# Optimization experiments

Hardware: AMD Instinct MI355X
Metric: run time of the kernel (lower is better)

## Reference

```python
import jax, jax.numpy as jnp
import numpy as np

# Multi-level grid resolutions (module constants from init_kwargs)
RESO_3D = [16, 32, 64]
RESO_2D = [64, 128, 256]
EPS = 1e-9


def _corners(D):
    # binary corner offsets, shape (2**D, D)
    c = np.stack(np.meshgrid(*([np.arange(2)] * D), indexing='ij'), axis=-1).reshape(-1, D)
    return jnp.asarray(c, dtype=jnp.int32)


def _coords_weights(xyz, reso):
    # xyz in [0,1), shape (N, D). Returns flat voxel idx (N, 2**D) and trilinear weights (N, 2**D).
    D = xyz.shape[1]
    corners = _corners(D)                                   # (C, D)
    x = xyz * (reso - 1)
    x0 = jnp.floor(x)
    frac = x - x0                                           # (N, D)
    x0 = x0.astype(jnp.int32)
    cc = jnp.clip(x0[:, None, :] + corners[None], 0, reso - 1)   # (N, C, D)
    w = jnp.prod(jnp.where(corners[None] == 1, frac[:, None, :], 1.0 - frac[:, None, :]), axis=-1)  # (N, C)
    strides = (reso ** jnp.arange(D - 1, -1, -1)).astype(jnp.int32)  # row-major
    idx = jnp.sum(cc * strides, axis=-1)                    # (N, C)
    return idx, w


def _grid_create(xyz, feat, reso):
    # Scatter-splat: weighted-average point features into a dense level grid (reso**D, F).
    N, D = xyz.shape
    F = feat.shape[1]
    idx, w = _coords_weights(xyz, reso)                     # (N, C)
    flat_idx = idx.reshape(-1)
    wf = jnp.zeros((reso ** D, F), dtype=feat.dtype).at[flat_idx].add(
        (w[..., None] * feat[:, None, :]).reshape(-1, F))
    ws = jnp.zeros((reso ** D,), dtype=feat.dtype).at[flat_idx].add(w.reshape(-1))
    return wf / jnp.maximum(ws, EPS)[:, None]


def _grid_encode(xyz, grid, reso):
    # Gather + trilinear interpolation from a dense level grid. Returns (M, F).
    idx, w = _coords_weights(xyz, reso)                     # (M, C)
    vals = grid[idx]                                        # (M, C, F)
    return jnp.sum(w[..., None] * vals, axis=1)


def _spatial_ctx(xyz_c, xyz_i, feat):
    outs = []
    # 3D multi-level grid
    for R in RESO_3D:
        g = _grid_create(xyz_c, feat, R)
        outs.append(_grid_encode(xyz_i, g, R))
    # triplane 2D grids: xy, xz, yz
    for dims in ((0, 1), (0, 2), (1, 2)):
        xc = xyz_c[:, list(dims)]
        xi = xyz_i[:, list(dims)]
        for R in RESO_2D:
            g = _grid_create(xc, feat, R)
            outs.append(_grid_encode(xi, g, R))
    return jnp.concatenate(outs, axis=-1)  # (M, (L3 + 3*L2) * F)


def setup_inputs() -> dict:
    key = jax.random.key(0)
    k1, k2, k3 = jax.random.split(key, 3)
    N, M, F = 200000, 100000, 32
    xyz_for_creater = jax.random.uniform(k1, (N, 3), dtype=jnp.float32)
    xyz_for_interp = jax.random.uniform(k2, (M, 3), dtype=jnp.float32)
    feature = jax.random.normal(k3, (N, F), dtype=jnp.float32)
    return {"xyz_for_creater": xyz_for_creater,
            "xyz_for_interp": xyz_for_interp,
            "feature": feature}


def reference(xyz_for_creater, xyz_for_interp, feature):
    return _spatial_ctx(xyz_for_creater, xyz_for_interp, feature)
```

## Files before the change

kernel.cpp:

```cpp
#include <hip/hip_runtime.h>

#define NF 32
#define EPSF 1e-9f

#define KSORT 458752
#define VO16 0
#define VO32 4096
#define VO64Q 36864
#define VO128Q 49152
#define KVIS2 98304
#define KO16 0
#define KO32 4096
#define KO64 36864
#define KO64Q 299008
#define KO128Q 311296
#define KO256Q 360448
#define KVIS 557056

__device__ __forceinline__ int cell_coord(float xv, int R, float& fr) {
  float x = xv * (float)(R - 1);
  int i0 = (int)floorf(x);
  i0 = min(max(i0, 0), R - 2);
  fr = x - (float)i0;
  return i0;
}
__device__ __forceinline__ float bf2f(unsigned short u) {
  return __uint_as_float((unsigned)u << 16);
}
__device__ __forceinline__ unsigned short f2bf(float x) {
  unsigned b = __float_as_uint(x);
  return (unsigned short)((b + 0x7FFF + ((b >> 16) & 1)) >> 16);
}
__device__ __forceinline__ unsigned p1b2(unsigned x) {
  x &= 0x3FF;
  x = (x | (x << 16)) & 0x030000FF;
  x = (x | (x << 8)) & 0x0300F00F;
  x = (x | (x << 4)) & 0x030C30C3;
  x = (x | (x << 2)) & 0x09249249;
  return x;
}
__device__ __forceinline__ unsigned p1b1(unsigned x) {
  x &= 0xFFFF;
  x = (x | (x << 8)) & 0x00FF00FF;
  x = (x | (x << 4)) & 0x0F0F0F0F;
  x = (x | (x << 2)) & 0x33333333;
  x = (x | (x << 1)) & 0x55555555;
  return x;
}
__device__ __forceinline__ unsigned c1b2(unsigned x) {
  x &= 0x09249249u;
  x = (x | (x >> 2)) & 0x030C30C3u;
  x = (x | (x >> 4)) & 0x0300F00Fu;
  x = (x | (x >> 8)) & 0x030000FFu;
  x = (x | (x >> 16)) & 0x3FFu;
  return x;
}
__device__ __forceinline__ unsigned c1b1(unsigned x) {
  x &= 0x55555555u;
  x = (x | (x >> 1)) & 0x33333333u;
  x = (x | (x >> 2)) & 0x0F0F0F0Fu;
  x = (x | (x >> 4)) & 0x00FF00FFu;
  x = (x | (x >> 8)) & 0xFFFFu;
  return x;
}

__device__ __forceinline__ int xcd_swz(int bid, int n) {
  return (bid & 7) * (n >> 3) + (bid >> 3);
}

__device__ __forceinline__ void agg_hist(int key, int* cnt) {
  int lane = threadIdx.x & 63;
  unsigned long long amask = __ballot(1);
  int nact = __popcll(amask);
  int prev = __shfl_up(key, 1);
  bool leader = (lane == 0) || (prev != key);
  unsigned long long lmask = __ballot(leader);
  if (leader) {
    unsigned long long above = (lane < 63) ? (lmask >> (lane + 1)) : 0ULL;
    int next = above ? (lane + 1 + (__ffsll((unsigned long long)above) - 1)) : nact;
    atomicAdd(&cnt[key], next - lane);
  }
}
template <int NC>
__device__ __forceinline__ void agg_place_batch(const int (&key)[NC], int* cur,
                                                int (&pos)[NC]) {
  int lane = threadIdx.x & 63;
  unsigned long long amask = __ballot(1);
  int nact = __popcll(amask);
  int ret[NC];
  int lp[NC];
#pragma unroll
  for (int c = 0; c < NC; ++c) {
    int prev = __shfl_up(key[c], 1);
    bool leader = (lane == 0) || (prev != key[c]);
    unsigned long long lmask = __ballot(leader);
    unsigned long long below = lmask & ((2ULL << lane) - 1ULL);
    lp[c] = 63 - __clzll((long long)below);
    ret[c] = 0;
    if (leader) {
      unsigned long long above = (lane < 63) ? (lmask >> (lane + 1)) : 0ULL;
      int next = above ? (lane + 1 + (__ffsll((unsigned long long)above) - 1)) : nact;
      ret[c] = atomicAdd(&cur[key[c]], next - lane);
    }
  }
#pragma unroll
  for (int c = 0; c < NC; ++c) pos[c] = __shfl(ret[c], lp[c]) + (lane - lp[c]);
}

__global__ __launch_bounds__(256) void sort_hist_all(
    const float* __restrict__ xyz, int* __restrict__ cnt, int N) {
  int p = blockIdx.x * blockDim.x + threadIdx.x;
  if (p >= N) return;
  float fr;
  int c64[3], c256[3];
#pragma unroll
  for (int d = 0; d < 3; ++d) {
    c64[d] = cell_coord(xyz[p * 3 + d], 64, fr);
    c256[d] = cell_coord(xyz[p * 3 + d], 256, fr);
  }
  int k3 = (int)((p1b2((unsigned)c64[0]) << 2) | (p1b2((unsigned)c64[1]) << 1) |
                 p1b2((unsigned)c64[2]));
  atomicAdd(&cnt[k3], 1);
#pragma unroll
  for (int g = 0; g < 3; ++g) {
    int a = (g < 2) ? 0 : 1, b = (g == 0) ? 1 : 2;
    int key = 262144 + g * 65536 +
              (int)((p1b1((unsigned)c256[a]) << 1) | p1b1((unsigned)c256[b]));
    atomicAdd(&cnt[key], 1);
  }
}
__global__ __launch_bounds__(256) void sort_place_all(
    const float* __restrict__ xyz, int* __restrict__ cur, int* __restrict__ perm, int N) {
  int p = blockIdx.x * blockDim.x + threadIdx.x;
  if (p >= N) return;
  float fr;
  int c64[3], c256[3];
#pragma unroll
  for (int d = 0; d < 3; ++d) {
    c64[d] = cell_coord(xyz[p * 3 + d], 64, fr);
    c256[d] = cell_coord(xyz[p * 3 + d], 256, fr);
  }
  int k3 = (int)((p1b2((unsigned)c64[0]) << 2) | (p1b2((unsigned)c64[1]) << 1) |
                 p1b2((unsigned)c64[2]));
  perm[atomicAdd(&cur[k3], 1)] = p;
#pragma unroll
  for (int g = 0; g < 3; ++g) {
    int a = (g < 2) ? 0 : 1, b = (g == 0) ? 1 : 2;
    int key = 262144 + g * 65536 +
              (int)((p1b1((unsigned)c256[a]) << 1) | p1b1((unsigned)c256[b]));
    perm[atomicAdd(&cur[key], 1)] = p;
  }
}
__global__ __launch_bounds__(256) void permute_all(
    const float* __restrict__ xyz, const float* __restrict__ feat,
    const int* __restrict__ perm, float* __restrict__ xyz_s,
    unsigned short* __restrict__ feat_s, float* __restrict__ xy_g,
    unsigned short* __restrict__ feat_g, int N) {
  int t = blockIdx.x * blockDim.x + threadIdx.x;
  int s = t >> 5, f = t & 31;
  if (s >= 4 * N) return;
  int q = perm[s];
  float v = feat[(size_t)q * NF + f];
  if (s < N) {
    feat_s[(size_t)s * NF + f] = f2bf(v);
    if (f < 3) xyz_s[s * 3 + f] = xyz[q * 3 + f];
  } else {
    int sl = s - N;
    int g = sl / N;
    feat_g[(size_t)sl * NF + f] = f2bf(v);
    if (f < 2) {
      int a = (g < 2) ? 0 : 1, b = (g == 0) ? 1 : 2;
      xy_g[(size_t)sl * 2 + f] = xyz[q * 3 + (f == 0 ? a : b)];
    }
  }
}

__global__ __launch_bounds__(256) void scan_blocksum(
    const int* __restrict__ cnt, int* __restrict__ bsum, int K) {
  __shared__ int red[256];
  int base = blockIdx.x * 2048 + threadIdx.x * 8;
  int s = 0;
#pragma unroll
  for (int j = 0; j < 8; ++j) {
    int k = base + j;
    if (k < K) s += cnt[k];
  }
  red[threadIdx.x] = s;
  __syncthreads();
  for (int off = 128; off > 0; off >>= 1) {
    if (threadIdx.x < off) red[threadIdx.x] += red[threadIdx.x + off];
    __syncthreads();
  }
  if (threadIdx.x == 0) bsum[blockIdx.x] = red[0];
}
__global__ __launch_bounds__(256) void scan_write(
    const int* __restrict__ cnt, const int* __restrict__ bsum,
    int* __restrict__ cur, int K) {
  __shared__ int lds[256];
  __shared__ int boff;
  int b = blockIdx.x, t = threadIdx.x;
  if (t == 0) {
    int s = 0;
    for (int j = 0; j < b; ++j) s += bsum[j];
    boff = s;
  }
  int base = b * 2048 + t * 8;
  int v[8];
  int s = 0;
#pragma unroll
  for (int j = 0; j < 8; ++j) {
    int k = base + j;
    v[j] = (k < K) ? cnt[k] : 0;
    s += v[j];
  }
  lds[t] = s;
  __syncthreads();
  for (int off = 1; off < 256; off <<= 1) {
    int add = (t >= off) ? lds[t - off] : 0;
    __syncthreads();
    lds[t] += add;
    __syncthreads();
  }
  int run = boff + lds[t] - s;
#pragma unroll
  for (int j = 0; j < 8; ++j) {
    int k = base + j;
    if (k < K) {
      cur[k] = run;
      run += v[j];
    }
  }
}

__global__ __launch_bounds__(256) void hist_fused(
    const float* __restrict__ xyz_s, const float* __restrict__ xy_g,
    int* __restrict__ cnt, int N) {
  int y = blockIdx.y;
  int p = blockIdx.x * blockDim.x + threadIdx.x;
  if (p >= N) return;
  if (y < 2) {
    int R = 16 << y;
    int ko = (y == 0) ? VO16 : VO32;
    unsigned a0[3], a1[3];
    float fr[3];
#pragma unroll
    for (int d = 0; d < 3; ++d) {
      int i0 = cell_coord(xyz_s[p * 3 + d], R, fr[d]);
      a0[d] = p1b2((unsigned)i0);
      a1[d] = p1b2((unsigned)(i0 + 1));
    }
#pragma unroll
    for (int cb = 0; cb < 8; ++cb) {
      unsigned key = 0;
#pragma unroll
      for (int d = 0; d < 3; ++d) {
        int o = (cb >> d) & 1;
        key |= (o ? a1[d] : a0[d]) << (2 - d);
      }
      agg_hist(ko + (int)key, cnt);
    }
  } else {
    int idx = y - 2;
    int g = idx >> 1, r = idx & 1;
    int sl = g * N + p;
    int R = 64 << r;
    int kb = (r == 0) ? VO64Q : VO128Q;
    int base = kb + g * R * R;
    float frx, fry;
    int ix = cell_coord(xy_g[(size_t)sl * 2 + 0], R, frx);
    int iy = cell_coord(xy_g[(size_t)sl * 2 + 1], R, fry);
    unsigned ax0 = p1b1((unsigned)ix), ax1 = p1b1((unsigned)(ix + 1));
    unsigned ay0 = p1b1((unsigned)iy), ay1 = p1b1((unsigned)(iy + 1));
#pragma unroll
    for (int cb = 0; cb < 4; ++cb) {
      int o0 = (cb >> 1) & 1, o1 = cb & 1;
      agg_hist(base + (int)(((o0 ? ax1 : ax0) << 1) | (o1 ? ay1 : ay0)), cnt);
    }
  }
}

__global__ __launch_bounds__(256) void place_fused(
    const float* __restrict__ xyz_s, const float* __restrict__ xy_g,
    int* __restrict__ cur_v, int2* __restrict__ visits, int N) {
  int y = blockIdx.y;
  int p = blockIdx.x * blockDim.x + threadIdx.x;
  if (p >= N) return;
  if (y < 2) {
    int R = 16 << y;
    int ko = (y == 0) ? VO16 : VO32;
    unsigned a0[3], a1[3];
    float fr[3];
#pragma unroll
    for (int d = 0; d < 3; ++d) {
      int i0 = cell_coord(xyz_s[p * 3 + d], R, fr[d]);
      a0[d] = p1b2((unsigned)i0);
      a1[d] = p1b2((unsigned)(i0 + 1));
    }
    int keys[8];
    float ws[8];
#pragma unroll
    for (int cb = 0; cb < 8; ++cb) {
      float w = 1.f;
      unsigned key = 0;
#pragma unroll
      for (int d = 0; d < 3; ++d) {
        int o = (cb >> d) & 1;
        w *= o ? fr[d] : (1.f - fr[d]);
        key |= (o ? a1[d] : a0[d]) << (2 - d);
      }
      keys[cb] = ko + (int)key;
      ws[cb] = w;
    }
    int pos[8];
    agg_place_batch<8>(keys, cur_v, pos);
#pragma unroll
    for (int cb = 0; cb < 8; ++cb)
      visits[pos[cb]] = make_int2(p, __float_as_int(ws[cb]));
  } else {
    int idx = y - 2;
    int g = idx >> 1, r = idx & 1;
    int sl = g * N + p;
    int R = 64 << r;
    int kb = (r == 0) ? VO64Q : VO128Q;
    int base = kb + g * R * R;
    float frx, fry;
    int ix = cell_coord(xy_g[(size_t)sl * 2 + 0], R, frx);
    int iy = cell_coord(xy_g[(size_t)sl * 2 + 1], R, fry);
    unsigned ax0 = p1b1((unsigned)ix), ax1 = p1b1((unsigned)(ix + 1));
    unsigned ay0 = p1b1((unsigned)iy), ay1 = p1b1((unsigned)(iy + 1));
    int keys[4];
    float ws[4];
#pragma unroll
    for (int cb = 0; cb < 4; ++cb) {
      int o0 = (cb >> 1) & 1, o1 = cb & 1;
      ws[cb] = (o0 ? frx : 1.f - frx) * (o1 ? fry : 1.f - fry);
      keys[cb] = base + (int)(((o0 ? ax1 : ax0) << 1) | (o1 ? ay1 : ay0));
    }
    int pos[4];
    agg_place_batch<4>(keys, cur_v, pos);
#pragma unroll
    for (int cb = 0; cb < 4; ++cb)
      visits[pos[cb]] = make_int2(sl, __float_as_int(ws[cb]));
  }
}

__global__ __launch_bounds__(256) void create_block_fused(
    const unsigned short* __restrict__ feat_s, const unsigned short* __restrict__ feat_g,
    const int* __restrict__ cnt, const int* __restrict__ cur_end,
    const int2* __restrict__ visits, unsigned short* __restrict__ grid) {
  __shared__ int2 vlds[1024];
  __shared__ float2 lacc[256];
  __shared__ float lw[16];
  int bid = blockIdx.x;
  int vo, go, base, nseg;
  const unsigned short* feat;
  if (bid < 4096) {
    vo = VO16; go = KO16; base = 0; nseg = 4096; feat = feat_s;
  } else if (bid < 36864) {
    vo = VO32; go = KO32; base = 4096; nseg = 32768; feat = feat_s;
  } else if (bid < 49152) {
    vo = VO64Q; go = KO64Q; base = 36864; nseg = 12288; feat = feat_g;
  } else {
    vo = VO128Q; go = KO128Q; base = 49152; nseg = 49152; feat = feat_g;
  }
  int idx = xcd_swz(bid - base, nseg);
  int vcell = vo + idx;
  int e = cur_end[vcell];
  int n = cnt[vcell];
  int beg = e - n;
  for (int i = threadIdx.x; i < n && i < 1024; i += 256) vlds[i] = visits[beg + i];
  __syncthreads();
  bool inl = (n <= 1024);
  int slot = threadIdx.x >> 4;
  int fp = threadIdx.x & 15;
  float2 acc = {0.f, 0.f};
  float wsum = 0.f;
  int i = slot;
  for (; i + 16 < n; i += 32) {
    int2 v0 = inl ? vlds[i] : visits[beg + i];
    int2 v1 = inl ? vlds[i + 16] : visits[beg + i + 16];
    unsigned u0 = *(const unsigned*)(feat + (size_t)v0.x * NF + 2 * fp);
    unsigned u1 = *(const unsigned*)(feat + (size_t)v1.x * NF + 2 * fp);
    float w0 = __int_as_float(v0.y), w1 = __int_as_float(v1.y);
    acc.x = fmaf(w0, bf2f((unsigned short)u0), acc.x);
    acc.y = fmaf(w0, bf2f((unsigned short)(u0 >> 16)), acc.y);
    acc.x = fmaf(w1, bf2f((unsigned short)u1), acc.x);
    acc.y = fmaf(w1, bf2f((unsigned short)(u1 >> 16)), acc.y);
    wsum += w0 + w1;
  }
  if (i < n) {
    int2 v = inl ? vlds[i] : visits[beg + i];
    unsigned u = *(const unsigned*)(feat + (size_t)v.x * NF + 2 * fp);
    float w = __int_as_float(v.y);
    acc.x = fmaf(w, bf2f((unsigned short)u), acc.x);
    acc.y = fmaf(w, bf2f((unsigned short)(u >> 16)), acc.y);
    wsum += w;
  }
  lacc[threadIdx.x] = acc;
  if (fp == 0) lw[slot] = wsum;
  __syncthreads();
  if (threadIdx.x < 16) {
    float2 a = {0.f, 0.f};
    float w = 0.f;
#pragma unroll
    for (int s = 0; s < 16; ++s) {
      float2 t = lacc[s * 16 + threadIdx.x];
      a.x += t.x;
      a.y += t.y;
      w += lw[s];
    }
    float inv = 1.f / fmaxf(w, EPSF);
    unsigned short lo = f2bf(a.x * inv), hi = f2bf(a.y * inv);
    *(unsigned*)(grid + (size_t)(go + idx) * NF + 2 * threadIdx.x) =
        (unsigned)lo | ((unsigned)hi << 16);
  }
}

__global__ __launch_bounds__(256) void create_direct_fused(
    const float* __restrict__ xyz_s, const unsigned short* __restrict__ feat_s,
    const float* __restrict__ xy_g, const unsigned short* __restrict__ feat_g,
    const int* __restrict__ cnt_all, const int* __restrict__ cur_all,
    unsigned short* __restrict__ grid, int N) {
  int bid = blockIdx.x;
  int wave = threadIdx.x >> 6, lane = threadIdx.x & 63;
  int slot = lane >> 4;
  int fp = lane & 15;
  float2 acc = {0.f, 0.f};
  float wsum = 0.f;
  int gcell;
  if (bid < 65536) {
    int cell = xcd_swz(bid, 65536) * 4 + wave;
    gcell = KO64 + cell;
    int cx = (int)c1b2((unsigned)cell >> 2);
    int cy = (int)c1b2((unsigned)cell >> 1);
    int cz = (int)c1b2((unsigned)cell);
    int beg[8], pre[8];
    int tot = 0;
#pragma unroll
    for (int cb = 0; cb < 8; ++cb) {
      pre[cb] = tot;
      int hx = cx - (cb & 1), hy = cy - ((cb >> 1) & 1), hz = cz - ((cb >> 2) & 1);
      int n = 0, b = 0;
      if (hx >= 0 && hy >= 0 && hz >= 0) {
        int hk = (int)((p1b2((unsigned)hx) << 2) | (p1b2((unsigned)hy) << 1) |
                       p1b2((unsigned)hz));
        n = cnt_all[hk];
        b = cur_all[hk] - n;
      }
      beg[cb] = b;
      tot += n;
    }
    for (int i = slot; i < tot; i += 4) {
      int cls = 0, b = beg[0], p0 = pre[0];
#pragma unroll
      for (int c2 = 1; c2 < 8; ++c2) {
        if (i >= pre[c2]) { cls = c2; b = beg[c2]; p0 = pre[c2]; }
      }
      int q = b + (i - p0);
      int hx = cx - (cls & 1), hy = cy - ((cls >> 1) & 1), hz = cz - ((cls >> 2) & 1);
      float frx = xyz_s[q * 3 + 0] * 63.0f - (float)hx;
      float fry = xyz_s[q * 3 + 1] * 63.0f - (float)hy;
      float frz = xyz_s[q * 3 + 2] * 63.0f - (float)hz;
      float w = ((cls & 1) ? frx : 1.f - frx) * (((cls >> 1) & 1) ? fry : 1.f - fry) *
                (((cls >> 2) & 1) ? frz : 1.f - frz);
      unsigned u = *(const unsigned*)(feat_s + (size_t)q * NF + 2 * fp);
      acc.x = fmaf(w, bf2f((unsigned short)u), acc.x);
      acc.y = fmaf(w, bf2f((unsigned short)(u >> 16)), acc.y);
      wsum += w;
    }
  } else {
    int cl = xcd_swz(bid - 65536, 49152) * 4 + wave;
    gcell = KO256Q + cl;
    int g = cl >> 16, m = cl & 65535;
    int cx = (int)c1b1((unsigned)m >> 1);
    int cy = (int)c1b1((unsigned)m);
    const int* cntg = cnt_all + 262144 + g * 65536;
    const int* curg = cur_all + 262144 + g * 65536;
    int beg[4], pre[4];
    int tot = 0;
#pragma unroll
    for (int cb = 0; cb < 4; ++cb) {
      pre[cb] = tot;
      int hx = cx - ((cb >> 1) & 1), hy = cy - (cb & 1);
      int n = 0, b = 0;
      if (hx >= 0 && hy >= 0) {
        int hk = (int)((p1b1((unsigned)hx) << 1) | p1b1((unsigned)hy));
        n = cntg[hk];
        b = curg[hk] - n - N;
      }
      beg[cb] = b;
      tot += n;
    }
    for (int i = slot; i < tot; i += 4) {
      int cls = 0, b = beg[0], p0 = pre[0];
#pragma unroll
      for (int c2 = 1; c2 < 4; ++c2) {
        if (i >= pre[c2]) { cls = c2; b = beg[c2]; p0 = pre[c2]; }
      }
      int q = b + (i - p0);
      int hx = cx - ((cls >> 1) & 1), hy = cy - (cls & 1);
      float frx = xy_g[(size_t)q * 2 + 0] * 255.0f - (float)hx;
      float fry = xy_g[(size_t)q * 2 + 1] * 255.0f - (float)hy;
      float w = (((cls >> 1) & 1) ? frx : 1.f - frx) * ((cls & 1) ? fry : 1.f - fry);
      unsigned u = *(const unsigned*)(feat_g + (size_t)q * NF + 2 * fp);
      acc.x = fmaf(w, bf2f((unsigned short)u), acc.x);
      acc.y = fmaf(w, bf2f((unsigned short)(u >> 16)), acc.y);
      wsum += w;
    }
  }
  acc.x += __shfl_xor(acc.x, 16);
  acc.y += __shfl_xor(acc.y, 16);
  wsum += __shfl_xor(wsum, 16);
  acc.x += __shfl_xor(acc.x, 32);
  acc.y += __shfl_xor(acc.y, 32);
  wsum += __shfl_xor(wsum, 32);
  if (slot == 0) {
    float inv = 1.f / fmaxf(wsum, EPSF);
    unsigned short lo = f2bf(acc.x * inv), hi = f2bf(acc.y * inv);
    *(unsigned*)(grid + (size_t)gcell * NF + 2 * fp) =
        (unsigned)lo | ((unsigned)hi << 16);
  }
}

__global__ __launch_bounds__(256) void encode_all(
    const float* __restrict__ xyz, const unsigned short* __restrict__ grid,
    float* __restrict__ out, int M) {
  int t = blockIdx.x * blockDim.x + threadIdx.x;
  int m = t >> 5, f = t & 31;
  if (m >= M) return;
  float X[3];
#pragma unroll
  for (int d = 0; d < 3; ++d) X[d] = xyz[m * 3 + d];
  {
    const int RS[3] = {16, 32, 64};
    const int KO[3] = {KO16, KO32, KO64};
#pragma unroll
    for (int r = 0; r < 3; ++r) {
      unsigned a0[3], a1[3];
      float fr[3];
#pragma unroll
      for (int d = 0; d < 3; ++d) {
        int i0 = cell_coord(X[d], RS[r], fr[d]);
        a0[d] = p1b2((unsigned)i0);
        a1[d] = p1b2((unsigned)(i0 + 1));
      }
      float acc = 0.f;
#pragma unroll
      for (int cb = 0; cb < 8; ++cb) {
        float w = 1.f;
        unsigned key = 0;
#pragma unroll
        for (int d = 0; d < 3; ++d) {
          int o = (cb >> d) & 1;
          w *= o ? fr[d] : (1.f - fr[d]);
          key |= (o ? a1[d] : a0[d]) << (2 - d);
        }
        acc = fmaf(w, bf2f(grid[(size_t)(KO[r] + (int)key) * NF + f]), acc);
      }
      out[(size_t)m * 384 + r * 32 + f] = acc;
    }
  }
  {
    const int RS[3] = {64, 128, 256};
    const int KB[3] = {KO64Q, KO128Q, KO256Q};
    const int RSQ[3] = {4096, 16384, 65536};
#pragma unroll
    for (int r = 0; r < 3; ++r) {
      unsigned b0[3], b1[3];
      float fr[3];
#pragma unroll
      for (int d = 0; d < 3; ++d) {
        int i0 = cell_coord(X[d], RS[r], fr[d]);
        b0[d] = p1b1((unsigned)i0);
        b1[d] = p1b1((unsigned)(i0 + 1));
      }
#pragma unroll
      for (int g = 0; g < 3; ++g) {
        int a = (g < 2) ? 0 : 1, b = (g == 0) ? 1 : 2;
        int base = KB[r] + g * RSQ[r];
        float acc = 0.f;
#pragma unroll
        for (int cb = 0; cb < 4; ++cb) {
          int o0 = (cb >> 1) & 1, o1 = cb & 1;
          float w = (o0 ? fr[a] : 1.f - fr[a]) * (o1 ? fr[b] : 1.f - fr[b]);
          int k = base + (int)(((o0 ? b1[a] : b0[a]) << 1) | (o1 ? b1[b] : b0[b]));
          acc = fmaf(w, bf2f(grid[(size_t)k * NF + f]), acc);
        }
        out[(size_t)m * 384 + (3 + g * 3 + r) * 32 + f] = acc;
      }
    }
  }
}

extern "C" void kernel_launch(void* const* d_in, const int* in_sizes, int n_in,
                              void* d_out, int out_size, void* d_ws, size_t ws_size,
                              hipStream_t stream) {
  const float* xyz_c = (const float*)d_in[0];
  const float* xyz_i = (const float*)d_in[1];
  const float* feat = (const float*)d_in[2];
  float* out = (float*)d_out;
  int N = in_sizes[0] / 3;
  int M = in_sizes[1] / 3;

  char* wsb = (char*)d_ws;
  size_t off = 0;
  auto al = [&](size_t bytes) {
    size_t o = off;
    off = (off + bytes + 255) & ~(size_t)255;
    return wsb + o;
  };
  const int KALL = KSORT + KVIS2;
  int* cnt_all = (int*)al((size_t)KALL * 4);
  int* cur_all = (int*)al((size_t)KALL * 4);
  int* bsum = (int*)al(4096);
  int* perm = (int*)al((size_t)4 * N * 4);
  float* xyz_s = (float*)al((size_t)N * 3 * 4);
  unsigned short* feat_s = (unsigned short*)al((size_t)N * NF * 2);
  float* xy_g = (float*)al((size_t)3 * N * 2 * 4);
  unsigned short* feat_g = (unsigned short*)al((size_t)3 * N * NF * 2);
  int2* visits = (int2*)al((size_t)40 * N * 8);
  unsigned short* grid = (unsigned short*)al((size_t)KVIS * NF * 2);

  int* cnt_v = cnt_all + KSORT;
  int* cur_v = cur_all + KSORT;

  int pb = (N + 255) / 256;
  int nbs = (KSORT + 2047) / 2048;
  int nbv = (KVIS2 + 2047) / 2048;

  hipMemsetAsync(cnt_all, 0, (size_t)KALL * 4, stream);

  sort_hist_all<<<pb, 256, 0, stream>>>(xyz_c, cnt_all, N);
  scan_blocksum<<<nbs, 256, 0, stream>>>(cnt_all, bsum, KSORT);
  scan_write<<<nbs, 256, 0, stream>>>(cnt_all, bsum, cur_all, KSORT);
  sort_place_all<<<pb, 256, 0, stream>>>(xyz_c, cur_all, perm, N);
  permute_all<<<(4 * N * 32 + 255) / 256, 256, 0, stream>>>(xyz_c, feat, perm, xyz_s,
                                                            feat_s, xy_g, feat_g, N);

  hist_fused<<<dim3(pb, 8), 256, 0, stream>>>(xyz_s, xy_g, cnt_v, N);
  scan_blocksum<<<nbv, 256, 0, stream>>>(cnt_v, bsum, KVIS2);
  scan_write<<<nbv, 256, 0, stream>>>(cnt_v, bsum, cur_v, KVIS2);
  place_fused<<<dim3(pb, 8), 256, 0, stream>>>(xyz_s, xy_g, cur_v, visits, N);

  create_block_fused<<<98304, 256, 0, stream>>>(feat_s, feat_g, cnt_v, cur_v, visits,
                                                grid);
  create_direct_fused<<<114688, 256, 0, stream>>>(xyz_s, feat_s, xy_g, feat_g, cnt_all,
                                                  cur_all, grid, N);

  encode_all<<<(M * 32 + 255) / 256, 256, 0, stream>>>(xyz_i, grid, out, M);
}
```

Baseline: 831.3 us.

## Replace per-cell gather splat with brick-tiled LDS scatter accumulation

```diff
diff --git a/kernel.cpp b/kernel.cpp
--- a/kernel.cpp
+++ b/kernel.cpp
@@ -416,109 +416,197 @@
   }
 }
 
-__global__ __launch_bounds__(256) void create_direct_fused(
+__global__ __launch_bounds__(256) void create_brick_fused(
     const float* __restrict__ xyz_s, const unsigned short* __restrict__ feat_s,
     const float* __restrict__ xy_g, const unsigned short* __restrict__ feat_g,
     const int* __restrict__ cnt_all, const int* __restrict__ cur_all,
     unsigned short* __restrict__ grid, int N) {
+  __shared__ float facc[8192];
+  __shared__ float fw[256];
+  __shared__ int2 blist[1024];
+  __shared__ int bcount;
+  int t = threadIdx.x;
+  for (int i = t; i < 8192; i += 256) facc[i] = 0.f;
+  fw[t] = 0.f;
+  if (t == 0) bcount = 0;
+  __syncthreads();
   int bid = blockIdx.x;
-  int wave = threadIdx.x >> 6, lane = threadIdx.x & 63;
-  int slot = lane >> 4;
-  int fp = lane & 15;
-  float2 acc = {0.f, 0.f};
-  float wsum = 0.f;
-  int gcell;
-  if (bid < 65536) {
-    int cell = xcd_swz(bid, 65536) * 4 + wave;
-    gcell = KO64 + cell;
-    int cx = (int)c1b2((unsigned)cell >> 2);
-    int cy = (int)c1b2((unsigned)cell >> 1);
-    int cz = (int)c1b2((unsigned)cell);
-    int beg[8], pre[8];
-    int tot = 0;
-#pragma unroll
-    for (int cb = 0; cb < 8; ++cb) {
-      pre[cb] = tot;
-      int hx = cx - (cb & 1), hy = cy - ((cb >> 1) & 1), hz = cz - ((cb >> 2) & 1);
-      int n = 0, b = 0;
-      if (hx >= 0 && hy >= 0 && hz >= 0) {
+  int f = t & 31, pg = t >> 5;
+  if (bid < 1024) {
+    int b = xcd_swz(bid, 1024);
+    int K = b << 8;
+    int bx = (int)c1b2((unsigned)K >> 2), by = (int)c1b2((unsigned)K >> 1),
+        bz = (int)c1b2((unsigned)K);
+    if (t < 149) {
+      int hx, hy, hz;
+      if (t < 81) {
+        hx = bx - 1; hy = by - 1 + t / 9; hz = bz - 1 + t % 9;
+      } else if (t < 117) {
+        int j = t - 81; hx = bx + j / 9; hy = by - 1; hz = bz - 1 + j % 9;
+      } else {
+        int j = t - 117; hx = bx + j / 8; hy = by + j % 8; hz = bz - 1;
+      }
+      if (hx >= 0 && hy >= 0 && hz >= 0 && hx < 64 && hy < 64 && hz < 64) {
         int hk = (int)((p1b2((unsigned)hx) << 2) | (p1b2((unsigned)hy) << 1) |
                        p1b2((unsigned)hz));
-        n = cnt_all[hk];
-        b = cur_all[hk] - n;
-      }
-      beg[cb] = b;
-      tot += n;
-    }
-    for (int i = slot; i < tot; i += 4) {
-      int cls = 0, b = beg[0], p0 = pre[0];
-#pragma unroll
-      for (int c2 = 1; c2 < 8; ++c2) {
-        if (i >= pre[c2]) { cls = c2; b = beg[c2]; p0 = pre[c2]; }
-      }
-      int q = b + (i - p0);
-      int hx = cx - (cls & 1), hy = cy - ((cls >> 1) & 1), hz = cz - ((cls >> 2) & 1);
-      float frx = xyz_s[q * 3 + 0] * 63.0f - (float)hx;
-      float fry = xyz_s[q * 3 + 1] * 63.0f - (float)hy;
-      float frz = xyz_s[q * 3 + 2] * 63.0f - (float)hz;
-      float w = ((cls & 1) ? frx : 1.f - frx) * (((cls >> 1) & 1) ? fry : 1.f - fry) *
-                (((cls >> 2) & 1) ? frz : 1.f - frz);
-      unsigned u = *(const unsigned*)(feat_s + (size_t)q * NF + 2 * fp);
-      acc.x = fmaf(w, bf2f((unsigned short)u), acc.x);
-      acc.y = fmaf(w, bf2f((unsigned short)(u >> 16)), acc.y);
-      wsum += w;
+        int n = cnt_all[hk];
+        if (n > 0) {
+          int st = cur_all[hk] - n;
+          int lb = atomicAdd(&bcount, n);
+          int pk = (hx - bx + 1) | ((hy - by + 1) << 8) | ((hz - bz + 1) << 16);
+          for (int i = 0; i < n; ++i)
+            if (lb + i < 1024) blist[lb + i] = make_int2(st + i, pk);
+        }
+      }
+    }
+    int S = cur_all[K] - cnt_all[K];
+    int E = cur_all[K + 255];
+    __syncthreads();
+    int nb = min(bcount, 1024);
+    for (int i = S + pg; i < E; i += 8) {
+      float x = xyz_s[i * 3 + 0] * 63.0f;
+      float y = xyz_s[i * 3 + 1] * 63.0f;
+      float z = xyz_s[i * 3 + 2] * 63.0f;
+      int hx = min(max((int)floorf(x), 0), 62);
+      int hy = min(max((int)floorf(y), 0), 62);
+      int hz = min(max((int)floorf(z), 0), 62);
+      float frx = x - (float)hx, fry = y - (float)hy, frz = z - (float)hz;
+      float fv = bf2f(feat_s[(size_t)i * NF + f]);
+      int lx0 = hx - bx, ly0 = hy - by, lz0 = hz - bz;
+#pragma unroll
+      for (int cb = 0; cb < 8; ++cb) {
+        int lx = lx0 + (cb & 1), ly = ly0 + ((cb >> 1) & 1), lz = lz0 + ((cb >> 2) & 1);
+        if ((unsigned)lx < 4u && (unsigned)ly < 8u && (unsigned)lz < 8u) {
+          float w = ((cb & 1) ? frx : 1.f - frx) *
+                    (((cb >> 1) & 1) ? fry : 1.f - fry) *
+                    (((cb >> 2) & 1) ? frz : 1.f - frz);
+          int lin = lx * 64 + ly * 8 + lz;
+          atomicAdd(&facc[lin * 32 + f], w * fv);
+          if (f == 0) atomicAdd(&fw[lin], w);
+        }
+      }
+    }
+    for (int i = pg; i < nb; i += 8) {
+      int2 e2 = blist[i];
+      int q = e2.x;
+      int dx = (e2.y & 255) - 1, dy = ((e2.y >> 8) & 255) - 1, dz = ((e2.y >> 16) & 255) - 1;
+      float x = xyz_s[q * 3 + 0] * 63.0f;
+      float y = xyz_s[q * 3 + 1] * 63.0f;
+      float z = xyz_s[q * 3 + 2] * 63.0f;
+      float frx = x - (float)(bx + dx), fry = y - (float)(by + dy),
+            frz = z - (float)(bz + dz);
+      float fv = bf2f(feat_s[(size_t)q * NF + f]);
+#pragma unroll
+      for (int cb = 0; cb < 8; ++cb) {
+        int lx = dx + (cb & 1), ly = dy + ((cb >> 1) & 1), lz = dz + ((cb >> 2) & 1);
+        if ((unsigned)lx < 4u && (unsigned)ly < 8u && (unsigned)lz < 8u) {
+          float w = ((cb & 1) ? frx : 1.f - frx) *
+                    (((cb >> 1) & 1) ? fry : 1.f - fry) *
+                    (((cb >> 2) & 1) ? frz : 1.f - frz);
+          int lin = lx * 64 + ly * 8 + lz;
+          atomicAdd(&facc[lin * 32 + f], w * fv);
+          if (f == 0) atomicAdd(&fw[lin], w);
+        }
+      }
+    }
+    __syncthreads();
+    size_t gb = (size_t)(KO64 + K) * NF;
+#pragma unroll
+    for (int it = 0; it < 16; ++it) {
+      int slot = it * 256 + t;
+      int cm = slot >> 4, fp = slot & 15;
+      int lz = (cm & 1) | ((cm >> 2) & 2) | ((cm >> 4) & 4);
+      int ly = ((cm >> 1) & 1) | ((cm >> 3) & 2) | ((cm >> 5) & 4);
+      int lx = ((cm >> 2) & 1) | ((cm >> 4) & 2);
+      int lin = lx * 64 + ly * 8 + lz;
+      float inv = 1.f / fmaxf(fw[lin], EPSF);
+      unsigned short lo = f2bf(facc[lin * 32 + 2 * fp] * inv);
+      unsigned short hi = f2bf(facc[lin * 32 + 2 * fp + 1] * inv);
+      *(unsigned*)(grid + gb + (size_t)cm * NF + 2 * fp) =
+          (unsigned)lo | ((unsigned)hi << 16);
     }
   } else {
-    int cl = xcd_swz(bid - 65536, 49152) * 4 + wave;
-    gcell = KO256Q + cl;
-    int g = cl >> 16, m = cl & 65535;
-    int cx = (int)c1b1((unsigned)m >> 1);
-    int cy = (int)c1b1((unsigned)m);
-    const int* cntg = cnt_all + 262144 + g * 65536;
-    const int* curg = cur_all + 262144 + g * 65536;
-    int beg[4], pre[4];
-    int tot = 0;
-#pragma unroll
-    for (int cb = 0; cb < 4; ++cb) {
-      pre[cb] = tot;
-      int hx = cx - ((cb >> 1) & 1), hy = cy - (cb & 1);
-      int n = 0, b = 0;
-      if (hx >= 0 && hy >= 0) {
-        int hk = (int)((p1b1((unsigned)hx) << 1) | p1b1((unsigned)hy));
-        n = cntg[hk];
-        b = curg[hk] - n - N;
-      }
-      beg[cb] = b;
-      tot += n;
-    }
-    for (int i = slot; i < tot; i += 4) {
-      int cls = 0, b = beg[0], p0 = pre[0];
-#pragma unroll
-      for (int c2 = 1; c2 < 4; ++c2) {
-        if (i >= pre[c2]) { cls = c2; b = beg[c2]; p0 = pre[c2]; }
-      }
-      int q = b + (i - p0);
-      int hx = cx - ((cls >> 1) & 1), hy = cy - (cls & 1);
-      float frx = xy_g[(size_t)q * 2 + 0] * 255.0f - (float)hx;
-      float fry = xy_g[(size_t)q * 2 + 1] * 255.0f - (float)hy;
-      float w = (((cls >> 1) & 1) ? frx : 1.f - frx) * ((cls & 1) ? fry : 1.f - fry);
-      unsigned u = *(const unsigned*)(feat_g + (size_t)q * NF + 2 * fp);
-      acc.x = fmaf(w, bf2f((unsigned short)u), acc.x);
-      acc.y = fmaf(w, bf2f((unsigned short)(u >> 16)), acc.y);
-      wsum += w;
-    }
-  }
-  acc.x += __shfl_xor(acc.x, 16);
-  acc.y += __shfl_xor(acc.y, 16);
-  wsum += __shfl_xor(wsum, 16);
-  acc.x += __shfl_xor(acc.x, 32);
-  acc.y += __shfl_xor(acc.y, 32);
-  wsum += __shfl_xor(wsum, 32);
-  if (slot == 0) {
-    float inv = 1.f / fmaxf(wsum, EPSF);
-    unsigned short lo = f2bf(acc.x * inv), hi = f2bf(acc.y * inv);
-    *(unsigned*)(grid + (size_t)gcell * NF + 2 * fp) =
-        (unsigned)lo | ((unsigned)hi << 16);
+    int b2 = xcd_swz(bid - 1024, 768);
+    int g = b2 >> 8, mb = b2 & 255;
+    int K0 = 262144 + g * 65536 + (mb << 8);
+    int bx = (int)c1b1((unsigned)(mb << 8) >> 1), by = (int)c1b1((unsigned)(mb << 8));
+    if (t < 33) {
+      int hx, hy;
+      if (t < 17) {
+        hx = bx - 1; hy = by - 1 + t;
+      } else {
+        hx = bx + (t - 17); hy = by - 1;
+      }
+      if (hx >= 0 && hy >= 0 && hx < 256 && hy < 256) {
+        int hk = 262144 + g * 65536 +
+                 (int)((p1b1((unsigned)hx) << 1) | p1b1((unsigned)hy));
+        int n = cnt_all[hk];
+        if (n > 0) {
+          int st = cur_all[hk] - n - N;
+          int lb = atomicAdd(&bcount, n);
+          int pk = (hx - bx + 1) | ((hy - by + 1) << 8);
+          for (int i = 0; i < n; ++i)
+            if (lb + i < 1024) blist[lb + i] = make_int2(st + i, pk);
+        }
+      }
+    }
+    int S = cur_all[K0] - cnt_all[K0] - N;
+    int E = cur_all[K0 + 255] - N;
+    __syncthreads();
+    int nb = min(bcount, 1024);
+    for (int i = S + pg; i < E; i += 8) {
+      float x = xy_g[(size_t)i * 2 + 0] * 255.0f;
+      float y = xy_g[(size_t)i * 2 + 1] * 255.0f;
+      int hx = min(max((int)floorf(x), 0), 254);
+      int hy = min(max((int)floorf(y), 0), 254);
+      float frx = x - (float)hx, fry = y - (float)hy;
+      float fv = bf2f(feat_g[(size_t)i * NF + f]);
+      int lx0 = hx - bx, ly0 = hy - by;
+#pragma unroll
+      for (int cb = 0; cb < 4; ++cb) {
+        int lx = lx0 + ((cb >> 1) & 1), ly = ly0 + (cb & 1);
+        if ((unsigned)lx < 16u && (unsigned)ly < 16u) {
+          float w = (((cb >> 1) & 1) ? frx : 1.f - frx) * ((cb & 1) ? fry : 1.f - fry);
+          int lin = lx * 16 + ly;
+          atomicAdd(&facc[lin * 32 + f], w * fv);
+          if (f == 0) atomicAdd(&fw[lin], w);
+        }
+      }
+    }
+    for (int i = pg; i < nb; i += 8) {
+      int2 e2 = blist[i];
+      int q = e2.x;
+      int dx = (e2.y & 255) - 1, dy = ((e2.y >> 8) & 255) - 1;
+      float x = xy_g[(size_t)q * 2 + 0] * 255.0f;
+      float y = xy_g[(size_t)q * 2 + 1] * 255.0f;
+      float frx = x - (float)(bx + dx), fry = y - (float)(by + dy);
+      float fv = bf2f(feat_g[(size_t)q * NF + f]);
+#pragma unroll
+      for (int cb = 0; cb < 4; ++cb) {
+        int lx = dx + ((cb >> 1) & 1), ly = dy + (cb & 1);
+        if ((unsigned)lx < 16u && (unsigned)ly < 16u) {
+          float w = (((cb >> 1) & 1) ? frx : 1.f - frx) * ((cb & 1) ? fry : 1.f - fry);
+          int lin = lx * 16 + ly;
+          atomicAdd(&facc[lin * 32 + f], w * fv);
+          if (f == 0) atomicAdd(&fw[lin], w);
+        }
+      }
+    }
+    __syncthreads();
+    size_t gb = (size_t)(KO256Q + g * 65536 + (mb << 8)) * NF;
+#pragma unroll
+    for (int it = 0; it < 16; ++it) {
+      int slot = it * 256 + t;
+      int cm = slot >> 4, fp = slot & 15;
+      int ly = (cm & 1) | ((cm >> 1) & 2) | ((cm >> 2) & 4) | ((cm >> 3) & 8);
+      int lx = ((cm >> 1) & 1) | ((cm >> 2) & 2) | ((cm >> 3) & 4) | ((cm >> 4) & 8);
+      int lin = lx * 16 + ly;
+      float inv = 1.f / fmaxf(fw[lin], EPSF);
+      unsigned short lo = f2bf(facc[lin * 32 + 2 * fp] * inv);
+      unsigned short hi = f2bf(facc[lin * 32 + 2 * fp + 1] * inv);
+      *(unsigned*)(grid + gb + (size_t)cm * NF + 2 * fp) =
+          (unsigned)lo | ((unsigned)hi << 16);
+    }
   }
 }
 
@@ -644,8 +732,8 @@
 
   create_block_fused<<<98304, 256, 0, stream>>>(feat_s, feat_g, cnt_v, cur_v, visits,
                                                 grid);
-  create_direct_fused<<<114688, 256, 0, stream>>>(xyz_s, feat_s, xy_g, feat_g, cnt_all,
-                                                  cur_all, grid, N);
+  create_brick_fused<<<1792, 256, 0, stream>>>(xyz_s, feat_s, xy_g, feat_g, cnt_all,
+                                               cur_all, grid, N);
 
   encode_all<<<(M * 32 + 255) / 256, 256, 0, stream>>>(xyz_i, grid, out, M);
 }
```

Result: slower. 1.319 ms (+58.6%).
